# Performance work log

Measured on AMD Instinct MI355X. Metric: run time of the kernel, lower is better.

The kernel has to match this reference:

```python
import jax, jax.numpy as jnp
import numpy as np
import math

T = 0.01      # temperature (init kwarg)
CUT = 32      # high-frequency cutoff (init kwarg)


def scalar_field(n, F):
    """Random scalar field of size [n,n] from the first m=F.shape[0] sine modes."""
    m = F.shape[0]
    xs = jnp.linspace(0.0, 1.0, n, dtype=F.dtype)
    k = jnp.arange(1, m + 1, dtype=F.dtype)
    i, j = jnp.meshgrid(k, k, indexing='ij')          # [m,m]
    r = jnp.sqrt(i * i + j * j)
    e = (r < m + 0.5).astype(F.dtype) / r             # sqrt(1/energy) mask
    s = jnp.sin(math.pi * xs[:, None] * k[None, :])   # [n,m]
    c = F * e
    return jnp.einsum('ij,xi,yj->yx', c, s, s)        # [n,n]


def remap_linear(a, dx, dy):
    """Bilinear remap of a [..., n, m] by displacement fields dx, dy of shape [n,m]."""
    n, m = a.shape[-2], a.shape[-1]
    dt = dx.dtype
    yy, xx = jnp.meshgrid(jnp.arange(n, dtype=dt), jnp.arange(m, dtype=dt), indexing='ij')
    xn = jnp.clip(xx + dx, 0, m - 1)
    yn = jnp.clip(yy + dy, 0, n - 1)
    xf = jnp.floor(xn).astype(jnp.int32)
    yf = jnp.floor(yn).astype(jnp.int32)
    xc = jnp.ceil(xn).astype(jnp.int32)
    yc = jnp.ceil(yn).astype(jnp.int32)
    xv = (xn - xf.astype(dt))[None, None]  # [1,1,n,m] broadcast over batch, channel
    yv = (yn - yf.astype(dt))[None, None]
    g = lambda yi, xi: a[..., yi, xi]      # gather corners -> [B,C,n,m]
    return ((1 - yv) * (1 - xv) * g(yf, xf)
            + (1 - yv) * xv * g(yf, xc)
            + yv * (1 - xv) * g(yc, xf)
            + yv * xv * g(yc, xc))


def setup_inputs() -> dict:
    key = jax.random.key(0)
    k1, k2, k3 = jax.random.split(key, 3)
    x = jax.random.normal(k1, (128, 3, 224, 224), dtype=jnp.float32)
    F_x = jax.random.normal(k2, (CUT, CUT), dtype=jnp.float32)
    F_y = jax.random.normal(k3, (CUT, CUT), dtype=jnp.float32)
    return {"x": x, "F_x": F_x, "F_y": F_y}


def reference(x, F_x, F_y):
    n = x.shape[-1]
    u = scalar_field(n, F_x)
    v = scalar_field(n, F_y)
    dx = (T ** 0.5) * u * n
    dy = (T ** 0.5) * v * n
    return remap_linear(x, dx, dy)
```

## Files before the change

kernel.cpp:

```cpp
#include <hip/hip_runtime.h>
#include <hip/hip_fp16.h>

#define N 224
#define M 32
#define NPIX (N * N)
#define NPLANE 384
#define PLT 128
#define NPGRP 3
#define TTILE 4704
#define NPT 6
#define RPX 64
#define NCHUNK (NPIX / RPX)
#define NXCD 8
#define CPX (NCHUNK / NXCD)
#define PI_F 3.14159265358979323846f

typedef float vfloat4 __attribute__((ext_vector_type(4)));
typedef float vfloat2 __attribute__((ext_vector_type(2)));

#define GLOAD16(gptr, lptr)                                                   \
    __builtin_amdgcn_global_load_lds(                                         \
        (const __attribute__((address_space(1))) void*)(gptr),                \
        (__attribute__((address_space(3))) void*)(lptr), 16, 0, 0)

__global__ __launch_bounds__(256) void fused_field_transpose(
    const float* __restrict__ x, const float* __restrict__ Fx,
    const float* __restrict__ Fy, int4* __restrict__ tab,
    __half* __restrict__ xt)
{
    const int tid = threadIdx.x;

    if (blockIdx.x < N) {
        __shared__ float cx[M][M];
        __shared__ float cy[M][M];
        __shared__ float sy[M];

        const int y = blockIdx.x;

        for (int idx = tid; idx < M * M; idx += 256) {
            const int i = idx / M, j = idx % M;
            const float fi = (float)(i + 1), fj = (float)(j + 1);
            const float r = sqrtf(fi * fi + fj * fj);
            const float e = (r < (float)M + 0.5f) ? (1.0f / r) : 0.0f;
            cx[i][j] = Fx[idx] * e;
            cy[i][j] = Fy[idx] * e;
        }
        if (tid < M) {
            const float ys = (float)y / (float)(N - 1);
            sy[tid] = sinf(PI_F * ys * (float)(tid + 1));
        }
        __syncthreads();

        if (tid >= N) return;
        const int xi = tid;

        float sx[M];
        const float xsv = (float)xi / (float)(N - 1);
#pragma unroll
        for (int i = 0; i < M; ++i)
            sx[i] = sinf(PI_F * xsv * (float)(i + 1));

        float u = 0.0f, v = 0.0f;
#pragma unroll 1
        for (int j = 0; j < M; ++j) {
            float tx = 0.0f, ty = 0.0f;
#pragma unroll
            for (int i = 0; i < M; ++i) {
                tx = fmaf(cx[i][j], sx[i], tx);
                ty = fmaf(cy[i][j], sx[i], ty);
            }
            const float syj = sy[j];
            u = fmaf(syj, tx, u);
            v = fmaf(syj, ty, v);
        }

        const float dxv = 22.4f * u;
        const float dyv = 22.4f * v;
        const float xn = fminf(fmaxf((float)xi + dxv, 0.0f), (float)(N - 1));
        const float yn = fminf(fmaxf((float)y + dyv, 0.0f), (float)(N - 1));
        const int bx = min((int)floorf(xn), N - 2);
        const int by = min((int)floorf(yn), N - 2);
        const float fx = xn - (float)bx;
        const float fy = yn - (float)by;

        tab[y * N + xi] = make_int4(by * N + bx,
                                    __float_as_int(fx), __float_as_int(fy), 0);
        return;
    }

    __shared__ float t[64 * 64];

    const int tb    = blockIdx.x - N;
    const int ptile = tb % NPT;
    const int xtile = tb / NPT;
    const int pl0   = ptile * 64;
    const int pix0  = xtile * 64;

    const int w  = tid >> 6;
    const int l  = tid & 63;
    const int r  = l >> 4;
    const int cp = l & 15;

#pragma unroll
    for (int i = 0; i < 4; ++i) {
        const int row0 = w * 16 + i * 4;
        const int f    = (row0 >> 2) & 15;
        const float* g = x + (size_t)(pl0 + row0 + r) * NPIX + pix0
                           + 4 * (cp ^ f);
        GLOAD16(g, &t[row0 * 64]);
    }
    __syncthreads();

    const int c = tid & 15;
    const int q = (tid >> 4) & 3;
    __half* xo = xt + (size_t)pix0 * NPLANE + pl0;
#pragma unroll
    for (int s = 0; s < 4; ++s) {
        const int P  = w * 16 + s * 4 + q;
        const int gc = (P >> 2) ^ c;
        const float f0 = t[(4 * c + 0) * 64 + gc * 4 + q];
        const float f1 = t[(4 * c + 1) * 64 + gc * 4 + q];
        const float f2 = t[(4 * c + 2) * 64 + gc * 4 + q];
        const float f3 = t[(4 * c + 3) * 64 + gc * 4 + q];
        union { uint2 u; __half2 hh[2]; } pk;
        pk.hh[0] = __floats2half2_rn(f0, f1);
        pk.hh[1] = __floats2half2_rn(f2, f3);
        *(uint2*)&xo[(size_t)P * NPLANE + 4 * c] = pk.u;
    }
}

__global__ __launch_bounds__(256) void remap_kernel(
    const __half* __restrict__ xt, const int4* __restrict__ tab,
    float* __restrict__ out)
{
    __shared__ float tile[RPX][130];
    __shared__ int4 ltab[RPX];

    const int tid = threadIdx.x;
    const int w = tid >> 6, l = tid & 63;

    const int bid   = blockIdx.x;
    const int xcd   = bid & 7;
    const int local = bid >> 3;
    const int pg    = local / CPX;
    const int chunk = xcd * CPX + (local % CPX);
    const int pix0  = chunk * RPX;

    if (tid < RPX) ltab[tid] = tab[pix0 + tid];
    __syncthreads();

    const __half2* base = (const __half2*)xt;
    const int pgoff = pg * (PLT / 2);

#pragma unroll 8
    for (int i = 0; i < 16; ++i) {
        const int pl = w * 16 + i;
        const int4 tb = ltab[pl];
        const float fx = __int_as_float(tb.y);
        const float fy = __int_as_float(tb.z);
        const float omx = 1.0f - fx, omy = 1.0f - fy;
        const float w00 = omy * omx, w01 = omy * fx;
        const float w10 = fy * omx,  w11 = fy * fx;

        const size_t b0 = (size_t)tb.x * (NPLANE / 2) + pgoff;
        const float2 c00 = __half22float2(base[b0 + l]);
        const float2 c01 = __half22float2(base[b0 + NPLANE / 2 + l]);
        const float2 c10 = __half22float2(base[b0 + (size_t)N * (NPLANE/2) + l]);
        const float2 c11 = __half22float2(base[b0 + (size_t)(N + 1) * (NPLANE/2) + l]);

        float2 o;
        o.x = w00 * c00.x + w01 * c01.x + w10 * c10.x + w11 * c11.x;
        o.y = w00 * c00.y + w01 * c01.y + w10 * c10.y + w11 * c11.y;
        *(float2*)&tile[pl][2 * l] = o;
    }
    __syncthreads();

    const int l2 = tid & 31, jg = tid >> 5;
    float* ob = out + (size_t)pg * PLT * NPIX + pix0;
#pragma unroll
    for (int s = 0; s < 16; ++s) {
        const int j = jg * 16 + s;
        vfloat2 o2;
        o2.x = tile[2 * l2][j];
        o2.y = tile[2 * l2 + 1][j];
        __builtin_nontemporal_store(o2, (vfloat2*)&ob[(size_t)j * NPIX + 2 * l2]);
    }
}

extern "C" void kernel_launch(void* const* d_in, const int* in_sizes, int n_in,
                              void* d_out, int out_size, void* d_ws, size_t ws_size,
                              hipStream_t stream) {
    const float* x  = (const float*)d_in[0];
    const float* Fx = (const float*)d_in[1];
    const float* Fy = (const float*)d_in[2];
    float* out = (float*)d_out;

    int4* tab = (int4*)d_ws;
    const size_t tab_bytes = (size_t)NPIX * sizeof(int4);
    __half* xt = (__half*)((char*)d_ws + tab_bytes);

    fused_field_transpose<<<N + TTILE, 256, 0, stream>>>(x, Fx, Fy, tab, xt);
    remap_kernel<<<NCHUNK * NPGRP, 256, 0, stream>>>(xt, tab, out);
}
```

Before: 48.60 us.

## Double-buffer transpose tiles so each block pipelines four pixel windows

The transpose part of the fused kernel now has each block handle four consecutive 64-pixel windows instead of one. It alternates two LDS buffers, issuing async global-to-LDS loads for the next window while the current one is converted to fp16 and stored, with manual vmcnt waits and barriers. The goal is to hide global load latency and cut per-block launch overhead. The cost is a larger shared allocation (32KB pool, shared with the field branch), which can lower occupancy, and fewer, longer blocks.

```diff
diff --git a/kernel.cpp b/kernel.cpp
--- a/kernel.cpp
+++ b/kernel.cpp
@@ -7,8 +7,10 @@
 #define NPLANE 384
 #define PLT 128
 #define NPGRP 3
-#define TTILE 4704
 #define NPT 6
+#define WPB 4
+#define NXG (784 / WPB)
+#define TBLK (NXG * NPT)
 #define RPX 64
 #define NCHUNK (NPIX / RPX)
 #define NXCD 8
@@ -28,12 +30,13 @@
     const float* __restrict__ Fy, int4* __restrict__ tab,
     __half* __restrict__ xt)
 {
+    __shared__ float pool[8192];
     const int tid = threadIdx.x;
 
     if (blockIdx.x < N) {
-        __shared__ float cx[M][M];
-        __shared__ float cy[M][M];
-        __shared__ float sy[M];
+        float* cx = pool;
+        float* cy = pool + M * M;
+        float* sy = pool + 2 * M * M;
 
         const int y = blockIdx.x;
 
@@ -42,8 +45,8 @@
             const float fi = (float)(i + 1), fj = (float)(j + 1);
             const float r = sqrtf(fi * fi + fj * fj);
             const float e = (r < (float)M + 0.5f) ? (1.0f / r) : 0.0f;
-            cx[i][j] = Fx[idx] * e;
-            cy[i][j] = Fy[idx] * e;
+            cx[idx] = Fx[idx] * e;
+            cy[idx] = Fy[idx] * e;
         }
         if (tid < M) {
             const float ys = (float)y / (float)(N - 1);
@@ -66,8 +69,8 @@
             float tx = 0.0f, ty = 0.0f;
 #pragma unroll
             for (int i = 0; i < M; ++i) {
-                tx = fmaf(cx[i][j], sx[i], tx);
-                ty = fmaf(cy[i][j], sx[i], ty);
+                tx = fmaf(cx[i * M + j], sx[i], tx);
+                ty = fmaf(cy[i * M + j], sx[i], ty);
             }
             const float syj = sy[j];
             u = fmaf(syj, tx, u);
@@ -88,45 +91,69 @@
         return;
     }
 
-    __shared__ float t[64 * 64];
+    float* const b0 = pool;
+    float* const b1 = pool + 4096;
 
     const int tb    = blockIdx.x - N;
     const int ptile = tb % NPT;
-    const int xtile = tb / NPT;
+    const int xg    = tb / NPT;
     const int pl0   = ptile * 64;
-    const int pix0  = xtile * 64;
 
     const int w  = tid >> 6;
     const int l  = tid & 63;
     const int r  = l >> 4;
     const int cp = l & 15;
-
-#pragma unroll
-    for (int i = 0; i < 4; ++i) {
-        const int row0 = w * 16 + i * 4;
-        const int f    = (row0 >> 2) & 15;
-        const float* g = x + (size_t)(pl0 + row0 + r) * NPIX + pix0
-                           + 4 * (cp ^ f);
-        GLOAD16(g, &t[row0 * 64]);
-    }
-    __syncthreads();
-
-    const int c = tid & 15;
-    const int q = (tid >> 4) & 3;
-    __half* xo = xt + (size_t)pix0 * NPLANE + pl0;
-#pragma unroll
-    for (int s = 0; s < 4; ++s) {
-        const int P  = w * 16 + s * 4 + q;
-        const int gc = (P >> 2) ^ c;
-        const float f0 = t[(4 * c + 0) * 64 + gc * 4 + q];
-        const float f1 = t[(4 * c + 1) * 64 + gc * 4 + q];
-        const float f2 = t[(4 * c + 2) * 64 + gc * 4 + q];
-        const float f3 = t[(4 * c + 3) * 64 + gc * 4 + q];
-        union { uint2 u; __half2 hh[2]; } pk;
-        pk.hh[0] = __floats2half2_rn(f0, f1);
-        pk.hh[1] = __floats2half2_rn(f2, f3);
-        *(uint2*)&xo[(size_t)P * NPLANE + 4 * c] = pk.u;
-    }
+    const int c  = tid & 15;
+    const int q  = (tid >> 4) & 3;
+
+#define ISSUE(win, bufp)                                                      \
+    do {                                                                      \
+        const int pix0_ = (xg * WPB + (win)) * 64;                            \
+        _Pragma("unroll")                                                     \
+        for (int i_ = 0; i_ < 4; ++i_) {                                      \
+            const int row0_ = w * 16 + i_ * 4;                                \
+            const int f_    = 4 * w + i_;                                     \
+            GLOAD16(x + (size_t)(pl0 + row0_ + r) * NPIX + pix0_              \
+                      + 4 * (cp ^ f_),                                        \
+                    (bufp) + row0_ * 64);                                     \
+        }                                                                     \
+    } while (0)
+
+    ISSUE(0, b0);
+    ISSUE(1, b1);
+
+#pragma unroll
+    for (int k = 0; k < WPB; ++k) {
+        asm volatile("s_waitcnt vmcnt(4)" ::: "memory");
+        __builtin_amdgcn_sched_barrier(0);
+        __builtin_amdgcn_s_barrier();
+        __builtin_amdgcn_sched_barrier(0);
+
+        const float* bufp = (k & 1) ? b1 : b0;
+        const int pix0 = (xg * WPB + k) * 64;
+        __half* xo = xt + (size_t)pix0 * NPLANE + pl0;
+#pragma unroll
+        for (int s = 0; s < 4; ++s) {
+            const int P  = w * 16 + s * 4 + q;
+            const int gc = (P >> 2) ^ c;
+            const float f0 = bufp[(4 * c + 0) * 64 + gc * 4 + q];
+            const float f1 = bufp[(4 * c + 1) * 64 + gc * 4 + q];
+            const float f2 = bufp[(4 * c + 2) * 64 + gc * 4 + q];
+            const float f3 = bufp[(4 * c + 3) * 64 + gc * 4 + q];
+            union { uint2 u; __half2 hh[2]; } pk;
+            pk.hh[0] = __floats2half2_rn(f0, f1);
+            pk.hh[1] = __floats2half2_rn(f2, f3);
+            *(uint2*)&xo[(size_t)P * NPLANE + 4 * c] = pk.u;
+        }
+
+        __builtin_amdgcn_sched_barrier(0);
+        __builtin_amdgcn_s_barrier();
+        __builtin_amdgcn_sched_barrier(0);
+
+        if (k == 0) ISSUE(2, b0);
+        if (k == 1) ISSUE(3, b1);
+    }
+#undef ISSUE
 }
 
 __global__ __launch_bounds__(256) void remap_kernel(
@@ -199,6 +226,6 @@
     const size_t tab_bytes = (size_t)NPIX * sizeof(int4);
     __half* xt = (__half*)((char*)d_ws + tab_bytes);
 
-    fused_field_transpose<<<N + TTILE, 256, 0, stream>>>(x, Fx, Fy, tab, xt);
+    fused_field_transpose<<<N + TBLK, 256, 0, stream>>>(x, Fx, Fy, tab, xt);
     remap_kernel<<<NCHUNK * NPGRP, 256, 0, stream>>>(xt, tab, out);
 }
```

Result: slower. 49.95 us (+2.8%).
